# Optimization experiments

Measured on AMD Instinct MI355X. Metric: run time of the kernel, lower is better.

Reference implementation:

```python
import jax, jax.numpy as jnp
import numpy as np

H = 256  # rnn hidden size

def _rnn_dir(x, wih, whh, bih, bhh):
    # x: [B,T,D] -> outputs [B,T,H]; h_t = tanh(x_t Wih^T + bih + h_{t-1} Whh^T + bhh)
    xproj = jnp.einsum('btd,hd->bth', x, wih) + bih + bhh  # precompute input projection
    def step(h, xp):
        h = jnp.tanh(xp + h @ whh.T)
        return h, h
    h0 = jnp.zeros((x.shape[0], whh.shape[0]), x.dtype)
    _, ys = jax.lax.scan(step, h0, jnp.swapaxes(xproj, 0, 1))
    return jnp.swapaxes(ys, 0, 1)

def _birnn(x, wif, whf, bif, bhf, wib, whb, bib, bhb):
    fwd = _rnn_dir(x, wif, whf, bif, bhf)
    bwd = _rnn_dir(x[:, ::-1, :], wib, whb, bib, bhb)[:, ::-1, :]
    return jnp.concatenate([fwd, bwd], axis=-1)

def setup_inputs() -> dict:
    key = jax.random.key(0)
    ks = jax.random.split(key, 24)
    B, T, V, E = 64, 512, 131072, 128
    s = 0.05
    emb = jax.random.normal(ks[0], (V, E), jnp.float32) * s
    emb = emb.at[0].set(0.0)  # padding_idx=0
    def W(k, shp):
        return jax.random.normal(k, shp, jnp.float32) * s
    inp = {
        'x': jax.random.randint(ks[1], (B, T), 0, V),
        'emb': emb,
        'r1_wif': W(ks[2], (H, E)), 'r1_whf': W(ks[3], (H, H)),
        'r1_bif': W(ks[4], (H,)), 'r1_bhf': W(ks[5], (H,)),
        'r1_wib': W(ks[6], (H, E)), 'r1_whb': W(ks[7], (H, H)),
        'r1_bib': W(ks[8], (H,)), 'r1_bhb': W(ks[9], (H,)),
        'r2_wif': W(ks[10], (H, 2 * H)), 'r2_whf': W(ks[11], (H, H)),
        'r2_bif': W(ks[12], (H,)), 'r2_bhf': W(ks[13], (H,)),
        'r2_wib': W(ks[14], (H, 2 * H)), 'r2_whb': W(ks[15], (H, H)),
        'r2_bib': W(ks[16], (H,)), 'r2_bhb': W(ks[17], (H,)),
        'ln_g': jnp.ones((1024,), jnp.float32),
        'ln_b': jnp.zeros((1024,), jnp.float32),
        'w1': W(ks[18], (512, 1024)), 'b1': W(ks[19], (512,)),
        'w2': W(ks[20], (256, 512)), 'b2': W(ks[21], (256,)),
    }
    return inp

def reference(x, emb, r1_wif, r1_whf, r1_bif, r1_bhf, r1_wib, r1_whb, r1_bib, r1_bhb,
              r2_wif, r2_whf, r2_bif, r2_bhf, r2_wib, r2_whb, r2_bib, r2_bhb,
              ln_g, ln_b, w1, b1, w2, b2):
    e = emb[x]  # [B,T,128]
    o1 = _birnn(e, r1_wif, r1_whf, r1_bif, r1_bhf, r1_wib, r1_whb, r1_bib, r1_bhb)  # [B,T,512]
    o2 = _birnn(o1, r2_wif, r2_whf, r2_bif, r2_bhf, r2_wib, r2_whb, r2_bib, r2_bhb)  # [B,T,512]
    last = o2[:, -1, :]
    mean = jnp.mean(o2, axis=1)
    h = jnp.concatenate([last, mean], axis=1)  # [B,1024]
    mu = jnp.mean(h, axis=-1, keepdims=True)
    var = jnp.mean(jnp.square(h - mu), axis=-1, keepdims=True)
    h = (h - mu) * jax.lax.rsqrt(var + 1e-5) * ln_g + ln_b
    h = jax.nn.relu(h @ w1.T + b1)
    return h @ w2.T + b2
```

## Files before the change

kernel.cpp:

```cpp
#include <hip/hip_runtime.h>
#include <stdint.h>

typedef unsigned short u16;
typedef unsigned int   u32;
typedef __attribute__((ext_vector_type(8))) short short8;
typedef __attribute__((ext_vector_type(4))) float f32x4;

#define T_LEN 512
#define HID   256

__device__ __forceinline__ float bflo(u32 u){ union{u32 i; float f;} v; v.i = u << 16; return v.f; }
__device__ __forceinline__ float bfhi(u32 u){ union{u32 i; float f;} v; v.i = u & 0xffff0000u; return v.f; }
__device__ __forceinline__ float b2f(u16 s){ union{u32 i; float f;} v; v.i = ((u32)s) << 16; return v.f; }
__device__ __forceinline__ u16 f2b(float f){
  union{float f; u32 i;} v; v.f = f;
  u32 r = v.i + 0x7fffu + ((v.i >> 16) & 1u);
  return (u16)(r >> 16);
}
__device__ __forceinline__ u32 pk2(float a, float b){ return (u32)f2b(a) | ((u32)f2b(b) << 16); }
__device__ __forceinline__ u32 cvtpk(float a, float b){
  u32 r; asm("v_cvt_pk_bf16_f32 %0, %1, %2" : "=v"(r) : "v"(a), "v"(b)); return r;
}
__device__ __forceinline__ float tanh_c(float x){
#if __has_builtin(__builtin_amdgcn_exp2f)
  float e = __builtin_amdgcn_exp2f(x * 2.885390081777927f);
#else
  float e = __expf(x + x);
#endif
  return __builtin_fmaf(-2.f, __builtin_amdgcn_rcpf(e + 1.f), 1.f);
}
__device__ __forceinline__ bool flag_bf16(const u32* f){ return (f[0] & 0xFFFFu) == 0x3F80u; }

#define NT 22
struct ConvArgs {
  const void* src[NT];
  u32 off[NT];
  u32 total;
  const u32* flagsrc;
};

__global__ __launch_bounds__(256)
void convert_params(ConvArgs a, u16* __restrict__ dst)
{
  const bool bf = flag_bf16(a.flagsrc);
  const u32 stride = gridDim.x * blockDim.x;
  for (u32 g = blockIdx.x * blockDim.x + threadIdx.x; g < a.total; g += stride) {
    int t = 0;
    #pragma unroll
    for (int i = 1; i < NT; ++i) t += (g >= a.off[i]);
    u32 local = g - a.off[t];
    dst[g] = bf ? ((const u16*)a.src[t])[local]
                : f2b(((const float*)a.src[t])[local]);
  }
}

template<int K, int SRC>
__global__ __launch_bounds__(256, 2)
void wgemm(const void* Bsrc, const int* __restrict__ gidx,
           const u16* __restrict__ Wf, const u16* __restrict__ Wb,
           const u16* __restrict__ bif, const u16* __restrict__ bhf,
           const u16* __restrict__ bib, const u16* __restrict__ bhb,
           u16* outT, const u32* flagsrc)
{
  __shared__ __align__(16) u16 lds[64 * K];
  const int tid  = threadIdx.x;
  const int row0 = blockIdx.x * 64;
  const int bb   = row0 >> 9;
  const int t0   = row0 & 511;
  const int bt   = bb >> 4, nb = bb & 15;
  constexpr int CPR = K / 8;

  bool abf = true;
  if (SRC == 0) abf = flag_bf16(flagsrc);

  for (int i = tid; i < 64 * CPR; i += 256) {
    int r = i / CPR, c = i % CPR;
    uint4 v;
    if (SRC == 0) {
      long rb = (long)gidx[row0 + r] * K;
      if (abf) {
        v = *(const uint4*)((const u16*)Bsrc + rb + c * 8);
      } else {
        const float* af = (const float*)Bsrc;
        float4 lo = *(const float4*)(af + rb + c * 8);
        float4 hi = *(const float4*)(af + rb + c * 8 + 4);
        v.x = pk2(lo.x, lo.y); v.y = pk2(lo.z, lo.w);
        v.z = pk2(hi.x, hi.y); v.w = pk2(hi.z, hi.w);
      }
    } else {
      int k = c * 8, d = k >> 8;
      size_t e = (size_t)(d * 4 + bt) * 2097152 + (size_t)(t0 + r) * 4096
               + (size_t)nb * 256 + (k & 255);
      v = *(const uint4*)((const u16*)Bsrc + e);
    }
    *(uint4*)&lds[r * K + ((c ^ (r & 7)) * 8)] = v;
  }
  __syncthreads();

  const int w = tid >> 6, lane = tid & 63, n16 = lane & 15, quad = lane >> 4;
  const int d = w >> 1;
  const u16* W  = d ? Wb : Wf;
  const u16* bi = d ? bib : bif;
  const u16* bh = d ? bhb : bhf;
  const int mbase = (w & 1) * 128;

  f32x4 acc[8][4];
  #pragma unroll
  for (int i = 0; i < 8; ++i)
    #pragma unroll
    for (int j = 0; j < 4; ++j) acc[i][j] = (f32x4){0.f, 0.f, 0.f, 0.f};

  #pragma unroll
  for (int kk = 0; kk < K / 32; ++kk) {
    short8 bfr[4];
    #pragma unroll
    for (int j = 0; j < 4; ++j) {
      int r = j * 16 + n16;
      int c = (kk * 4 + quad) ^ (r & 7);
      bfr[j] = *(const short8*)&lds[r * K + c * 8];
    }
    #pragma unroll
    for (int i = 0; i < 8; ++i) {
      short8 afr = *(const short8*)(W + (size_t)(mbase + i * 16 + n16) * K + kk * 32 + quad * 8);
      #pragma unroll
      for (int j = 0; j < 4; ++j)
        acc[i][j] = __builtin_amdgcn_mfma_f32_16x16x32_bf16(afr, bfr[j], acc[i][j], 0, 0, 0);
    }
  }

  #pragma unroll
  for (int i = 0; i < 8; ++i) {
    int mrow0 = mbase + i * 16 + quad * 4;
    uint2 biv = *(const uint2*)(bi + mrow0);
    uint2 bhv = *(const uint2*)(bh + mrow0);
    float bias0 = b2f(biv.x & 0xffff) + b2f(bhv.x & 0xffff);
    float bias1 = b2f(biv.x >> 16)    + b2f(bhv.x >> 16);
    float bias2 = b2f(biv.y & 0xffff) + b2f(bhv.y & 0xffff);
    float bias3 = b2f(biv.y >> 16)    + b2f(bhv.y >> 16);
    #pragma unroll
    for (int j = 0; j < 4; ++j) {
      int t = t0 + j * 16 + n16;
      uint2 pv;
      pv.x = pk2(acc[i][j][0] + bias0, acc[i][j][1] + bias1);
      pv.y = pk2(acc[i][j][2] + bias2, acc[i][j][3] + bias3);
      size_t e = (size_t)(d * 4 + bt) * 2097152 + (size_t)t * 4096
               + (size_t)nb * 256 + mrow0;
      *(uint2*)(outT + e) = pv;
    }
  }
}

template<int MODE>
__device__ __forceinline__ void scan_step4(
    int s, int send,
    const u16* hrp,
    u16* hwp,
    uint2 (&pf)[2],
    const u16*& xptr, u16*& optr, int pstep,
    const short8 (&wa)[2][8], f32x4 (&sum)[2], float* lastb, int lbase)
{
  uint2 xv0 = pf[0], xv1 = pf[1];
  pf[0] = *(const uint2*)(xptr);
  pf[1] = *(const uint2*)(xptr + 16);
  xptr += pstep;

  short8 hb[8];
  #pragma unroll
  for (int kk = 0; kk < 8; ++kk)
    hb[kk] = *(const short8*)(hrp + kk * 32);

  f32x4 a0 = (f32x4){bflo(xv0.x), bfhi(xv0.x), bflo(xv0.y), bfhi(xv0.y)};
  f32x4 a1 = (f32x4){bflo(xv1.x), bfhi(xv1.x), bflo(xv1.y), bfhi(xv1.y)};
  f32x4 b0 = (f32x4){0.f, 0.f, 0.f, 0.f};
  f32x4 b1 = (f32x4){0.f, 0.f, 0.f, 0.f};
  #pragma unroll
  for (int kk = 0; kk < 8; kk += 2) {
    a0 = __builtin_amdgcn_mfma_f32_16x16x32_bf16(wa[0][kk],     hb[kk],     a0, 0, 0, 0);
    a1 = __builtin_amdgcn_mfma_f32_16x16x32_bf16(wa[1][kk],     hb[kk],     a1, 0, 0, 0);
    b0 = __builtin_amdgcn_mfma_f32_16x16x32_bf16(wa[0][kk + 1], hb[kk + 1], b0, 0, 0, 0);
    b1 = __builtin_amdgcn_mfma_f32_16x16x32_bf16(wa[1][kk + 1], hb[kk + 1], b1, 0, 0, 0);
  }

  float h00 = tanh_c(a0[0] + b0[0]), h01 = tanh_c(a0[1] + b0[1]);
  float h02 = tanh_c(a0[2] + b0[2]), h03 = tanh_c(a0[3] + b0[3]);
  float h10 = tanh_c(a1[0] + b1[0]), h11 = tanh_c(a1[1] + b1[1]);
  float h12 = tanh_c(a1[2] + b1[2]), h13 = tanh_c(a1[3] + b1[3]);

  uint2 hv0; hv0.x = cvtpk(h00, h01); hv0.y = cvtpk(h02, h03);
  uint2 hv1; hv1.x = cvtpk(h10, h11); hv1.y = cvtpk(h12, h13);
  *(uint2*)(hwp)      = hv0;
  *(uint2*)(hwp + 16) = hv1;

  if (MODE == 0) {
    *(uint2*)(optr)      = hv0;
    *(uint2*)(optr + 16) = hv1;
    optr += pstep;
  } else {
    sum[0] += (f32x4){h00, h01, h02, h03};
    sum[1] += (f32x4){h10, h11, h12, h13};
    if (s == send) {
      *(float4*)&lastb[lbase]      = (float4){h00, h01, h02, h03};
      *(float4*)&lastb[lbase + 16] = (float4){h10, h11, h12, h13};
    }
  }

  asm volatile("s_waitcnt lgkmcnt(0)" ::: "memory");
  __builtin_amdgcn_s_barrier();
  asm volatile("" ::: "memory");
}

template<int MODE>
__global__ __launch_bounds__(512, 1)
void rnn_scan(const u16* xpT,
              const u16* __restrict__ whhF, const u16* __restrict__ whhB,
              u16* o1T, float* __restrict__ lastb, float* __restrict__ sumb)
{
  __shared__ __align__(16) u16 hl[2][16][264];
  const int tid = threadIdx.x, w = tid >> 6, lane = tid & 63;
  const int n16 = lane & 15, quad = lane >> 4;
  const int dir = blockIdx.x >> 2, bt = blockIdx.x & 3;
  const u16* whh = dir ? whhB : whhF;

  short8 wa[2][8];
  #pragma unroll
  for (int j = 0; j < 2; ++j)
    #pragma unroll
    for (int kk = 0; kk < 8; ++kk)
      wa[j][kk] = *(const short8*)(whh + (size_t)(w * 32 + j * 16 + n16) * 256
                                       + kk * 32 + quad * 8);

  for (int i = tid; i < 16 * 264; i += 512) ((u16*)hl[0])[i] = 0;

  const size_t blkbase = (size_t)(dir * 4 + bt) * 2097152;
  const int t0    = dir ? 511 : 0;
  const int pstep = dir ? -4096 : 4096;
  const int m0    = w * 32 + quad * 4;
  const u16* xptr = xpT + blkbase + (size_t)t0 * 4096 + n16 * 256 + m0;
  u16*       optr = o1T + blkbase + (size_t)t0 * 4096 + n16 * 256 + m0;
  const int lbase = (dir * 64 + bt * 16 + n16) * 256 + m0;
  const int send  = dir ? 0 : 511;

  const u16* hr0 = &hl[0][n16][quad * 8];
  const u16* hr1 = &hl[1][n16][quad * 8];
  u16* hw0 = &hl[1][n16][m0];
  u16* hw1 = &hl[0][n16][m0];

  uint2 pf0[2], pf1[2];
  pf0[0] = *(const uint2*)(xptr);
  pf0[1] = *(const uint2*)(xptr + 16);
  xptr += pstep;
  pf1[0] = *(const uint2*)(xptr);
  pf1[1] = *(const uint2*)(xptr + 16);
  xptr += pstep;

  f32x4 sum[2];
  sum[0] = (f32x4){0.f, 0.f, 0.f, 0.f};
  sum[1] = (f32x4){0.f, 0.f, 0.f, 0.f};
  __syncthreads();

  for (int s = 0; s < 512; s += 2) {
    scan_step4<MODE>(s,     send, hr0, hw0, pf0, xptr, optr, pstep, wa, sum, lastb, lbase);
    scan_step4<MODE>(s + 1, send, hr1, hw1, pf1, xptr, optr, pstep, wa, sum, lastb, lbase);
  }

  if (MODE == 1) {
    *(float4*)&sumb[lbase]      = (float4){sum[0][0], sum[0][1], sum[0][2], sum[0][3]};
    *(float4*)&sumb[lbase + 16] = (float4){sum[1][0], sum[1][1], sum[1][2], sum[1][3]};
  }
}

__device__ __forceinline__ float dot8(uint4 q, const float* hp){
  return bflo(q.x)*hp[0] + bfhi(q.x)*hp[1] + bflo(q.y)*hp[2] + bfhi(q.y)*hp[3]
       + bflo(q.z)*hp[4] + bfhi(q.z)*hp[5] + bflo(q.w)*hp[6] + bfhi(q.w)*hp[7];
}

__global__ __launch_bounds__(256)
void head_kernel(const float* __restrict__ lastb, const float* __restrict__ sumb,
                 const u16* __restrict__ g, const u16* __restrict__ be,
                 const u16* __restrict__ w1, const u16* __restrict__ b1,
                 const u16* __restrict__ w2, const u16* __restrict__ b2,
                 void* outv, const u32* flagsrc)
{
  __shared__ __align__(16) float hv[1024];
  __shared__ __align__(16) float act[512];
  __shared__ float red[8];
  const int tid = threadIdx.x;
  const int b   = blockIdx.x;
  const bool bf = flag_bf16(flagsrc);

  float v0 = lastb[b * 256 + tid];
  float v1 = lastb[(64 + b) * 256 + tid];
  float v2 = sumb[b * 256 + tid] * (1.f / 512.f);
  float v3 = sumb[(64 + b) * 256 + tid] * (1.f / 512.f);
  hv[tid] = v0; hv[256 + tid] = v1; hv[512 + tid] = v2; hv[768 + tid] = v3;

  float s  = v0 + v1 + v2 + v3;
  float ss = v0*v0 + v1*v1 + v2*v2 + v3*v3;
  #pragma unroll
  for (int off = 32; off; off >>= 1) {
    s  += __shfl_down(s, off);
    ss += __shfl_down(ss, off);
  }
  if ((tid & 63) == 0) { red[tid >> 6] = s; red[4 + (tid >> 6)] = ss; }
  __syncthreads();
  float S  = red[0] + red[1] + red[2] + red[3];
  float SS = red[4] + red[5] + red[6] + red[7];
  float mu   = S * (1.f / 1024.f);
  float var  = SS * (1.f / 1024.f) - mu * mu;
  float rstd = rsqrtf(var + 1e-5f);

  #pragma unroll
  for (int i = 0; i < 4; ++i) {
    int idx = i * 256 + tid;
    hv[idx] = (hv[idx] - mu) * rstd * b2f(g[idx]) + b2f(be[idx]);
  }
  __syncthreads();

  #pragma unroll
  for (int jj = 0; jj < 2; ++jj) {
    int j = jj * 256 + tid;
    const uint4* wr = (const uint4*)(w1 + (long)j * 1024);
    float a = 0.f;
    for (int c = 0; c < 128; ++c) a += dot8(wr[c], &hv[c * 8]);
    a += b2f(b1[j]);
    act[j] = a > 0.f ? a : 0.f;
  }
  __syncthreads();

  const uint4* wr2 = (const uint4*)(w2 + (long)tid * 512);
  float a = 0.f;
  for (int c = 0; c < 64; ++c) a += dot8(wr2[c], &act[c * 8]);
  a += b2f(b2[tid]);

  if (bf) {
    ((u16*)outv)[b * 256 + tid] = f2b(a);
  } else {
    union { u32 i; float f; } u; u.i = ((u32)f2b(a)) << 16;
    ((float*)outv)[b * 256 + tid] = u.f;
  }
}

extern "C" void kernel_launch(void* const* d_in, const int* in_sizes, int n_in,
                              void* d_out, int out_size, void* d_ws, size_t ws_size,
                              hipStream_t stream)
{
  const int* x    = (const int*)d_in[0];
  const u32* flag = (const u32*)d_in[18];

  static const int sizes[NT] = {
    32768, 65536, 256, 256, 32768, 65536, 256, 256,
    131072, 65536, 256, 256, 131072, 65536, 256, 256,
    1024, 1024, 524288, 512, 131072, 256
  };
  ConvArgs ca;
  u32 off = 0;
  for (int i = 0; i < NT; ++i) {
    ca.src[i] = d_in[2 + i];
    ca.off[i] = off;
    off += (u32)sizes[i];
  }
  ca.total = off;
  ca.flagsrc = flag;

  char* ws = (char*)d_ws;
  u16*   buf    = (u16*)ws;
  u16*   pm     = (u16*)(ws + 33554432);
  float* lastb  = (float*)(ws + 36054528);
  float* sumb   = (float*)(ws + 36185600);

  const u16* p_r1wif = pm + 0;
  const u16* p_r1whf = pm + 32768;
  const u16* p_r1bif = pm + 98304;
  const u16* p_r1bhf = pm + 98560;
  const u16* p_r1wib = pm + 98816;
  const u16* p_r1whb = pm + 131584;
  const u16* p_r1bib = pm + 197120;
  const u16* p_r1bhb = pm + 197376;
  const u16* p_r2wif = pm + 197632;
  const u16* p_r2whf = pm + 328704;
  const u16* p_r2bif = pm + 394240;
  const u16* p_r2bhf = pm + 394496;
  const u16* p_r2wib = pm + 394752;
  const u16* p_r2whb = pm + 525824;
  const u16* p_r2bib = pm + 591360;
  const u16* p_r2bhb = pm + 591616;
  const u16* p_lng   = pm + 591872;
  const u16* p_lnb   = pm + 592896;
  const u16* p_w1    = pm + 593920;
  const u16* p_b1    = pm + 1118208;
  const u16* p_w2    = pm + 1118720;
  const u16* p_b2    = pm + 1249792;

  convert_params<<<1024, 256, 0, stream>>>(ca, pm);

  wgemm<128, 0><<<512, 256, 0, stream>>>(d_in[1], x,
      p_r1wif, p_r1wib, p_r1bif, p_r1bhf, p_r1bib, p_r1bhb, buf, flag);
  rnn_scan<0><<<8, 512, 0, stream>>>(buf, p_r1whf, p_r1whb, buf, nullptr, nullptr);
  wgemm<512, 1><<<512, 256, 0, stream>>>(buf, nullptr,
      p_r2wif, p_r2wib, p_r2bif, p_r2bhf, p_r2bib, p_r2bhb, buf, flag);
  rnn_scan<1><<<8, 512, 0, stream>>>(buf, p_r2whf, p_r2whb, nullptr, lastb, sumb);
  head_kernel<<<64, 256, 0, stream>>>(lastb, sumb, p_lng, p_lnb, p_w1, p_b1, p_w2, p_b2,
      d_out, flag);
}
```

Baseline: 1.008 ms.

## Fold tanh exponent scale into weights and stagger per-wave LDS read order

Pre-scales the recurrent weights and the input projection by 2/ln2 so the scan's tanh needs no multiply before exp2. Rotates the k-chunk order per wave so the eight waves read different LDS banks of the hidden state at the same time. Splits the two MFMA chains so the first half's tanh and LDS write can start earlier, and raises wave priority around the MFMAs. Also changes launch bounds to allow two blocks per CU, which may constrain registers. Storing the pre-scaled projection in bf16 slightly changes rounding.

Result: faster. 915.4 us (-9.2%).

```diff
diff --git a/kernel.cpp b/kernel.cpp
--- a/kernel.cpp
+++ b/kernel.cpp
@@ -8,6 +8,8 @@
 
 #define T_LEN 512
 #define HID   256
+#define C2LE 2.8853900817779268f
+#define BUFOFF 4224
 
 __device__ __forceinline__ float bflo(u32 u){ union{u32 i; float f;} v; v.i = u << 16; return v.f; }
 __device__ __forceinline__ float bfhi(u32 u){ union{u32 i; float f;} v; v.i = u & 0xffff0000u; return v.f; }
@@ -21,11 +23,11 @@
 __device__ __forceinline__ u32 cvtpk(float a, float b){
   u32 r; asm("v_cvt_pk_bf16_f32 %0, %1, %2" : "=v"(r) : "v"(a), "v"(b)); return r;
 }
-__device__ __forceinline__ float tanh_c(float x){
+__device__ __forceinline__ float tanh_pre(float y){
 #if __has_builtin(__builtin_amdgcn_exp2f)
-  float e = __builtin_amdgcn_exp2f(x * 2.885390081777927f);
+  float e = __builtin_amdgcn_exp2f(y);
 #else
-  float e = __expf(x + x);
+  float e = exp2f(y);
 #endif
   return __builtin_fmaf(-2.f, __builtin_amdgcn_rcpf(e + 1.f), 1.f);
 }
@@ -49,8 +51,10 @@
     #pragma unroll
     for (int i = 1; i < NT; ++i) t += (g >= a.off[i]);
     u32 local = g - a.off[t];
-    dst[g] = bf ? ((const u16*)a.src[t])[local]
-                : f2b(((const float*)a.src[t])[local]);
+    float v = bf ? b2f(((const u16*)a.src[t])[local])
+                 : ((const float*)a.src[t])[local];
+    if (t == 1 || t == 5 || t == 9 || t == 13) v *= C2LE;
+    dst[g] = f2b(v);
   }
 }
 
@@ -141,8 +145,8 @@
     for (int j = 0; j < 4; ++j) {
       int t = t0 + j * 16 + n16;
       uint2 pv;
-      pv.x = pk2(acc[i][j][0] + bias0, acc[i][j][1] + bias1);
-      pv.y = pk2(acc[i][j][2] + bias2, acc[i][j][3] + bias3);
+      pv.x = cvtpk(C2LE * (acc[i][j][0] + bias0), C2LE * (acc[i][j][1] + bias1));
+      pv.y = cvtpk(C2LE * (acc[i][j][2] + bias2), C2LE * (acc[i][j][3] + bias3));
       size_t e = (size_t)(d * 4 + bt) * 2097152 + (size_t)t * 4096
                + (size_t)nb * 256 + mrow0;
       *(uint2*)(outT + e) = pv;
@@ -150,15 +154,17 @@
   }
 }
 
-template<int MODE>
-__device__ __forceinline__ void scan_step4(
+template<int MODE, int RDOFF>
+__device__ __forceinline__ void scan_step7(
     int s, int send,
-    const u16* hrp,
-    u16* hwp,
+    u16* const (&ra)[8],
+    u16* hwb,
     uint2 (&pf)[2],
     const u16*& xptr, u16*& optr, int pstep,
     const short8 (&wa)[2][8], f32x4 (&sum)[2], float* lastb, int lbase)
 {
+  constexpr int WROFF = RDOFF ^ BUFOFF;
+
   uint2 xv0 = pf[0], xv1 = pf[1];
   pf[0] = *(const uint2*)(xptr);
   pf[1] = *(const uint2*)(xptr + 16);
@@ -166,30 +172,35 @@
 
   short8 hb[8];
   #pragma unroll
-  for (int kk = 0; kk < 8; ++kk)
-    hb[kk] = *(const short8*)(hrp + kk * 32);
-
+  for (int c = 0; c < 8; ++c)
+    hb[c] = *(const short8*)(ra[c] + RDOFF);
+
+  __builtin_amdgcn_s_setprio(1);
   f32x4 a0 = (f32x4){bflo(xv0.x), bfhi(xv0.x), bflo(xv0.y), bfhi(xv0.y)};
+  f32x4 b0 = (f32x4){0.f, 0.f, 0.f, 0.f};
+  #pragma unroll
+  for (int c = 0; c < 8; c += 2) {
+    a0 = __builtin_amdgcn_mfma_f32_16x16x32_bf16(wa[0][c],     hb[c],     a0, 0, 0, 0);
+    b0 = __builtin_amdgcn_mfma_f32_16x16x32_bf16(wa[0][c + 1], hb[c + 1], b0, 0, 0, 0);
+  }
   f32x4 a1 = (f32x4){bflo(xv1.x), bfhi(xv1.x), bflo(xv1.y), bfhi(xv1.y)};
-  f32x4 b0 = (f32x4){0.f, 0.f, 0.f, 0.f};
   f32x4 b1 = (f32x4){0.f, 0.f, 0.f, 0.f};
   #pragma unroll
-  for (int kk = 0; kk < 8; kk += 2) {
-    a0 = __builtin_amdgcn_mfma_f32_16x16x32_bf16(wa[0][kk],     hb[kk],     a0, 0, 0, 0);
-    a1 = __builtin_amdgcn_mfma_f32_16x16x32_bf16(wa[1][kk],     hb[kk],     a1, 0, 0, 0);
-    b0 = __builtin_amdgcn_mfma_f32_16x16x32_bf16(wa[0][kk + 1], hb[kk + 1], b0, 0, 0, 0);
-    b1 = __builtin_amdgcn_mfma_f32_16x16x32_bf16(wa[1][kk + 1], hb[kk + 1], b1, 0, 0, 0);
-  }
-
-  float h00 = tanh_c(a0[0] + b0[0]), h01 = tanh_c(a0[1] + b0[1]);
-  float h02 = tanh_c(a0[2] + b0[2]), h03 = tanh_c(a0[3] + b0[3]);
-  float h10 = tanh_c(a1[0] + b1[0]), h11 = tanh_c(a1[1] + b1[1]);
-  float h12 = tanh_c(a1[2] + b1[2]), h13 = tanh_c(a1[3] + b1[3]);
-
+  for (int c = 0; c < 8; c += 2) {
+    a1 = __builtin_amdgcn_mfma_f32_16x16x32_bf16(wa[1][c],     hb[c],     a1, 0, 0, 0);
+    b1 = __builtin_amdgcn_mfma_f32_16x16x32_bf16(wa[1][c + 1], hb[c + 1], b1, 0, 0, 0);
+  }
+  __builtin_amdgcn_s_setprio(0);
+
+  float h00 = tanh_pre(a0[0] + b0[0]), h01 = tanh_pre(a0[1] + b0[1]);
+  float h02 = tanh_pre(a0[2] + b0[2]), h03 = tanh_pre(a0[3] + b0[3]);
   uint2 hv0; hv0.x = cvtpk(h00, h01); hv0.y = cvtpk(h02, h03);
+  *(uint2*)(hwb + WROFF) = hv0;
+
+  float h10 = tanh_pre(a1[0] + b1[0]), h11 = tanh_pre(a1[1] + b1[1]);
+  float h12 = tanh_pre(a1[2] + b1[2]), h13 = tanh_pre(a1[3] + b1[3]);
   uint2 hv1; hv1.x = cvtpk(h10, h11); hv1.y = cvtpk(h12, h13);
-  *(uint2*)(hwp)      = hv0;
-  *(uint2*)(hwp + 16) = hv1;
+  *(uint2*)(hwb + WROFF + 16) = hv1;
 
   if (MODE == 0) {
     *(uint2*)(optr)      = hv0;
@@ -210,7 +221,7 @@
 }
 
 template<int MODE>
-__global__ __launch_bounds__(512, 1)
+__global__ __launch_bounds__(512, 2)
 void rnn_scan(const u16* xpT,
               const u16* __restrict__ whhF, const u16* __restrict__ whhB,
               u16* o1T, float* __restrict__ lastb, float* __restrict__ sumb)
@@ -220,30 +231,35 @@
   const int n16 = lane & 15, quad = lane >> 4;
   const int dir = blockIdx.x >> 2, bt = blockIdx.x & 3;
   const u16* whh = dir ? whhB : whhF;
+  const int m0 = w * 32 + quad * 4;
 
   short8 wa[2][8];
   #pragma unroll
   for (int j = 0; j < 2; ++j)
     #pragma unroll
-    for (int kk = 0; kk < 8; ++kk)
-      wa[j][kk] = *(const short8*)(whh + (size_t)(w * 32 + j * 16 + n16) * 256
+    for (int c = 0; c < 8; ++c) {
+      int kk = (c + w) & 7;
+      wa[j][c] = *(const short8*)(whh + (size_t)(w * 32 + j * 16 + n16) * 256
                                        + kk * 32 + quad * 8);
+    }
+
+  u16* ra[8];
+  #pragma unroll
+  for (int c = 0; c < 8; ++c) {
+    int kk = (c + w) & 7;
+    ra[c] = &hl[0][n16][kk * 32 + quad * 8];
+  }
+  u16* hwb = &hl[0][n16][m0];
 
   for (int i = tid; i < 16 * 264; i += 512) ((u16*)hl[0])[i] = 0;
 
   const size_t blkbase = (size_t)(dir * 4 + bt) * 2097152;
   const int t0    = dir ? 511 : 0;
   const int pstep = dir ? -4096 : 4096;
-  const int m0    = w * 32 + quad * 4;
   const u16* xptr = xpT + blkbase + (size_t)t0 * 4096 + n16 * 256 + m0;
   u16*       optr = o1T + blkbase + (size_t)t0 * 4096 + n16 * 256 + m0;
   const int lbase = (dir * 64 + bt * 16 + n16) * 256 + m0;
   const int send  = dir ? 0 : 511;
-
-  const u16* hr0 = &hl[0][n16][quad * 8];
-  const u16* hr1 = &hl[1][n16][quad * 8];
-  u16* hw0 = &hl[1][n16][m0];
-  u16* hw1 = &hl[0][n16][m0];
 
   uint2 pf0[2], pf1[2];
   pf0[0] = *(const uint2*)(xptr);
@@ -259,8 +275,8 @@
   __syncthreads();
 
   for (int s = 0; s < 512; s += 2) {
-    scan_step4<MODE>(s,     send, hr0, hw0, pf0, xptr, optr, pstep, wa, sum, lastb, lbase);
-    scan_step4<MODE>(s + 1, send, hr1, hw1, pf1, xptr, optr, pstep, wa, sum, lastb, lbase);
+    scan_step7<MODE, 0>     (s,     send, ra, hwb, pf0, xptr, optr, pstep, wa, sum, lastb, lbase);
+    scan_step7<MODE, BUFOFF>(s + 1, send, ra, hwb, pf1, xptr, optr, pstep, wa, sum, lastb, lbase);
   }
 
   if (MODE == 1) {
```
